# Performance work log

Measured on AMD Instinct MI355X. Metric: run time of the kernel, lower is better.

The kernel has to match this reference:

```python
import jax, jax.numpy as jnp
import numpy as np

B, T, D = 8, 512, 1024
H, DQK, DV = 16, 128, 128  # n_heads, d_qk = emb_dim//h_qk, d_v = emb_dim//h_v


def setup_inputs() -> dict:
    key = jax.random.key(0)
    ks = jax.random.split(key, 8)
    s = 0.02
    return {
        "X": jax.random.normal(ks[0], (B, T, D), jnp.float32),
        "pos_enc_k": jax.random.normal(ks[1], (T, T, DQK), jnp.float32) * s,
        "pos_enc_v": jax.random.normal(ks[2], (T, T, DV), jnp.float32) * s,
        "Wq": jax.random.normal(ks[3], (D, H * DQK), jnp.float32) * s,
        "bq": jnp.zeros((H * DQK,), jnp.float32),
        "Wk": jax.random.normal(ks[4], (D, H * DQK), jnp.float32) * s,
        "bk": jnp.zeros((H * DQK,), jnp.float32),
        "Wv": jax.random.normal(ks[5], (D, H * DV), jnp.float32) * s,
        "bv": jnp.zeros((H * DV,), jnp.float32),
        "Wp": jax.random.normal(ks[6], (H * DV, D), jnp.float32) * s,
        "bp": jnp.zeros((D,), jnp.float32),
    }


def reference(X, pos_enc_k, pos_enc_v, Wq, bq, Wk, bk, Wv, bv, Wp, bp):
    b, t, d = X.shape
    # projections -> (b, h, t, dhead)
    Q = (X @ Wq + bq).reshape(b, t, H, DQK).transpose(0, 2, 1, 3)
    K = (X @ Wk + bk).reshape(b, t, H, DQK).transpose(0, 2, 1, 3)
    V = (X @ Wv + bv).reshape(b, t, H, DV).transpose(0, 2, 1, 3)
    # content attention + relative-position key bias
    att = jnp.einsum("bhqd,bhkd->bhqk", Q, K)
    att = att + jnp.einsum("bhqd,qkd->bhqk", Q, pos_enc_k)
    att = att / jnp.sqrt(jnp.asarray(DQK, X.dtype))
    # causal mask (do_mask=True)
    causal = jnp.tril(jnp.ones((t, t), bool))
    att = jnp.where(causal[None, None], att, jnp.asarray(-jnp.inf, att.dtype))
    att = jax.nn.softmax(att, axis=-1)
    # values + relative-position value correction
    y = jnp.einsum("bhqk,bhkd->bhqd", att, V)
    y = y + jnp.einsum("bhqk,qkd->bhqd", att, pos_enc_v)
    y = y.transpose(0, 2, 1, 3).reshape(b, t, H * DV)
    return y @ Wp + bp
```

## Files before the change

### kernel.cpp

```cpp
#include <hip/hip_runtime.h>
#include <stdint.h>

#define B_  8
#define T_  512
#define D_  1024
#define H_  16
#define DH  128
#define BH  128
#define ND  2048
#define BT  4096

typedef __attribute__((ext_vector_type(8))) short          short8;
typedef __attribute__((ext_vector_type(8))) __bf16         bf16x8;
typedef __attribute__((ext_vector_type(4))) float          f32x4;
typedef __attribute__((ext_vector_type(4))) unsigned short ushort4v;

static __device__ __forceinline__ unsigned short f2bf(float f) {
  unsigned u = __builtin_bit_cast(unsigned, f);
  u += 0x7FFFu + ((u >> 16) & 1u);
  return (unsigned short)(u >> 16);
}
static __device__ __forceinline__ float bf2f(unsigned short h) {
  unsigned u = ((unsigned)h) << 16;
  return __builtin_bit_cast(float, u);
}
static __device__ __forceinline__ f32x4 mfma16(short8 a, short8 b, f32x4 c) {
  return __builtin_amdgcn_mfma_f32_16x16x32_bf16(
      __builtin_bit_cast(bf16x8, a), __builtin_bit_cast(bf16x8, b), c, 0, 0, 0);
}
static __device__ __forceinline__ void gload16(const unsigned short* g, unsigned short* l) {
  __builtin_amdgcn_global_load_lds(
      (const __attribute__((address_space(1))) void*)g,
      (__attribute__((address_space(3))) void*)l, 16, 0, 0);
}

template <int ROWS, int COLS>
static __device__ __forceinline__ void stage_gl2(unsigned short* lds,
                                                 const unsigned short* __restrict__ src,
                                                 long stride, int tid) {
  constexpr int CPR = COLS / 8;
#pragma unroll
  for (int it = 0; it < ROWS * COLS / 8 / 256; ++it) {
    int chunk = tid + it * 256;
    int r = chunk / CPR, c8 = (chunk % CPR) * 8;
    gload16(src + (long)r * stride + c8, lds + chunk * 8);
  }
}

template <int ROWS>
static __device__ __forceinline__ void stage_sw64(unsigned short* lds,
                                                  const unsigned short* __restrict__ src,
                                                  long stride, int tid) {
#pragma unroll
  for (int it = 0; it < ROWS / 32; ++it) {
    int n = tid + it * 256;
    int r = n >> 3, c = (n & 7) ^ (r & 7);
    gload16(src + (long)r * stride + c * 8, lds + n * 8);
  }
}

template <int MR, int NR>
static __device__ __forceinline__ void mfma_sw64(const unsigned short* As,
                                                 const unsigned short* Bs,
                                                 int a0, int b0, int lrow, int g,
                                                 f32x4 (*acc)[NR]) {
#pragma unroll
  for (int ks = 0; ks < 2; ++ks) {
    short8 a[MR], b[NR];
#pragma unroll
    for (int i = 0; i < MR; ++i) {
      int ra = a0 + i * 16 + lrow;
      int c = (ks * 4 + g) ^ (ra & 7);
      a[i] = *(const short8*)&As[ra * 64 + c * 8];
    }
#pragma unroll
    for (int j = 0; j < NR; ++j) {
      int rb = b0 + j * 16 + lrow;
      int c = (ks * 4 + g) ^ (rb & 7);
      b[j] = *(const short8*)&Bs[rb * 64 + c * 8];
    }
#pragma unroll
    for (int i = 0; i < MR; ++i)
#pragma unroll
      for (int j = 0; j < NR; ++j) acc[i][j] = mfma16(a[i], b[j], acc[i][j]);
  }
}

#define IDS4                             \
  const int tid  = threadIdx.x;          \
  const int lane = tid & 63;             \
  const int wid  = tid >> 6;             \
  const int lrow = lane & 15;            \
  const int lk8  = (lane >> 4) * 8;      \
  const int lr4  = (lane >> 4) * 4;      \
  const int lg   = lane >> 4;            \
  const int wm = wid >> 1, wn = wid & 1;

#define LTS 132
#define LTQ 68

__global__ __launch_bounds__(256) void k_prep(const float* __restrict__ X,
                                              unsigned short* __restrict__ Xb,
                                              const float* __restrict__ Wq,
                                              const float* __restrict__ Wk,
                                              const float* __restrict__ Wv,
                                              const float* __restrict__ Wp,
                                              unsigned short* __restrict__ WT,
                                              unsigned short* __restrict__ WpT) {
  __shared__ float tile[32][33];
  int bid = blockIdx.x;
  if (bid < 4096) {
    int i = bid * 256 + threadIdx.x;
    f32x4 v = ((const f32x4*)X)[i];
    ushort4v o;
    o.x = f2bf(v.x); o.y = f2bf(v.y); o.z = f2bf(v.z); o.w = f2bf(v.w);
    ((ushort4v*)Xb)[i] = o;
    return;
  }
  bid -= 4096;
  const int which = bid >> 11;
  const int local = bid & 2047;
  const float* in;
  unsigned short* outp;
  int R, C, bx, by;
  if (which < 3) {
    in = which == 0 ? Wq : (which == 1 ? Wk : Wv);
    outp = WT + (size_t)which * ND * D_;
    R = D_; C = ND; bx = local & 63; by = local >> 6;
  } else {
    in = Wp; outp = WpT;
    R = ND; C = D_; bx = local & 31; by = local >> 5;
  }
  int c0 = bx * 32, r0 = by * 32;
  int tx = threadIdx.x & 31, ty = threadIdx.x >> 5;
#pragma unroll
  for (int i = 0; i < 32; i += 8)
    tile[ty + i][tx] = in[(long)(r0 + ty + i) * C + (c0 + tx)];
  __syncthreads();
#pragma unroll
  for (int i = 0; i < 32; i += 8)
    outp[(long)(c0 + ty + i) * R + (r0 + tx)] = f2bf(tile[tx][ty + i]);
}

__global__ __launch_bounds__(256) void k_proj8(const unsigned short* __restrict__ Xb,
                                               const unsigned short* __restrict__ WT,
                                               const float* __restrict__ bq,
                                               const float* __restrict__ bk,
                                               const float* __restrict__ bv,
                                               unsigned short* __restrict__ Qb,
                                               unsigned short* __restrict__ Kb,
                                               unsigned short* __restrict__ Vt) {
  __shared__ unsigned short As[128 * 64], Bs[128 * 64];
  IDS4
  const int flat = blockIdx.x, xcd = flat & 7, local = flat >> 3;
  const int nt = xcd * 6 + (local % 6);
  const int mt = local / 6;
  const int m0 = mt * 128, n0 = nt * 128;

  f32x4 acc[4][4] = {};
  for (int kk = 0; kk < D_; kk += 64) {
    stage_sw64<128>(As, Xb + (long)m0 * D_ + kk, D_, tid);
    stage_sw64<128>(Bs, WT + (long)n0 * D_ + kk, D_, tid);
    __syncthreads();
    mfma_sw64<4, 4>(As, Bs, wm * 64, wn * 64, lrow, lg, acc);
    __syncthreads();
  }

  const int nb = n0 >> 11;
  const float* biasp = nb == 0 ? bq : (nb == 1 ? bk : bv);
  const int hcol = (n0 & 2047) >> 7;
  if (nb < 2) {
    unsigned short* dst = nb == 0 ? Qb : Kb;
#pragma unroll
    for (int i = 0; i < 4; ++i)
#pragma unroll
      for (int j = 0; j < 4; ++j) {
        int cc = (n0 & 2047) + wn * 64 + j * 16 + lrow;
        int dd = cc & 127;
        float bias = biasp[cc];
#pragma unroll
        for (int r = 0; r < 4; ++r) {
          int m = m0 + wm * 64 + i * 16 + lr4 + r;
          int bb = m >> 9, tt = m & (T_ - 1);
          dst[((long)(bb * H_ + hcol) * T_ + tt) * DH + dd] = f2bf(acc[i][j][r] + bias);
        }
      }
  } else {
#pragma unroll
    for (int i = 0; i < 4; ++i)
#pragma unroll
      for (int j = 0; j < 4; ++j) {
        int cc = (n0 & 2047) + wn * 64 + j * 16 + lrow;
        int dd = cc & 127;
        float bias = biasp[cc];
#pragma unroll
        for (int r = 0; r < 4; ++r) {
          int m = m0 + wm * 64 + i * 16 + lr4 + r;
          int bb = m >> 9, tt = m & (T_ - 1);
          Vt[((long)(bb * H_ + hcol) * DH + dd) * T_ + tt] = f2bf(acc[i][j][r] + bias);
        }
      }
  }
}

__global__ __launch_bounds__(256) void k_posk(const unsigned short* __restrict__ Qb,
                                              const float* __restrict__ Pk,
                                              unsigned short* __restrict__ att) {
  const int bid = blockIdx.x;
  const int q = (bid & 1) ? (T_ - 1 - (bid >> 1)) : (bid >> 1);
  const int ktiles = (q >> 6) + 1;
  __shared__ unsigned short As[128 * 128];
  __shared__ unsigned short Bs[2][64 * 136];
  IDS4
  {
    const unsigned short* src = Qb + (long)q * DH;
#pragma unroll
    for (int it = 0; it < 8; ++it) {
      int n = tid + it * 256;
      int r = n >> 4, c = (n & 15) ^ (r & 7);
      gload16(src + (long)r * (T_ * DH) + c * 8, As + n * 8);
    }
  }
  f32x4 pv[8];
  const float* psrc = Pk + (long)q * T_ * DH;
  auto loadPk = [&](int kt) {
#pragma unroll
    for (int it = 0; it < 8; ++it) {
      int chunk = tid + it * 256;
      int r = chunk >> 5, c4 = (chunk & 31) * 4;
      pv[it] = *(const f32x4*)(psrc + (long)(kt * 64 + r) * DH + c4);
    }
  };
  auto writeB = [&](int buf) {
#pragma unroll
    for (int it = 0; it < 8; ++it) {
      int chunk = tid + it * 256;
      int r = chunk >> 5, c4 = (chunk & 31) * 4;
      ushort4v o;
      o.x = f2bf(pv[it].x); o.y = f2bf(pv[it].y); o.z = f2bf(pv[it].z); o.w = f2bf(pv[it].w);
      *(ushort4v*)&Bs[buf][r * 136 + c4] = o;
    }
  };
  loadPk(0);
  asm volatile("s_waitcnt vmcnt(0)" ::: "memory");
  writeB(0);
  asm volatile("s_waitcnt lgkmcnt(0)" ::: "memory");
  __builtin_amdgcn_s_barrier();
  for (int kt = 0; kt < ktiles; ++kt) {
    const bool pre = (kt + 1 < ktiles);
    if (pre) loadPk(kt + 1);
    f32x4 acc[4][2] = {};
#pragma unroll
    for (int ks = 0; ks < 4; ++ks) {
      short8 a[4], b[2];
#pragma unroll
      for (int i = 0; i < 4; ++i) {
        int ra = wm * 64 + i * 16 + lrow;
        int c = (ks * 4 + lg) ^ (ra & 7);
        a[i] = *(const short8*)&As[ra * 128 + c * 8];
      }
#pragma unroll
      for (int j = 0; j < 2; ++j)
        b[j] = *(const short8*)&Bs[kt & 1][(wn * 32 + j * 16 + lrow) * 136 + ks * 32 + lk8];
#pragma unroll
      for (int i = 0; i < 4; ++i)
#pragma unroll
        for (int j = 0; j < 2; ++j)
          acc[i][j] = mfma16(a[i], b[j], acc[i][j]);
    }
    if (pre) {
      asm volatile("s_waitcnt vmcnt(0)" ::: "memory");
      writeB((kt + 1) & 1);
    }
#pragma unroll
    for (int i = 0; i < 4; ++i)
#pragma unroll
      for (int j = 0; j < 2; ++j) {
        int k = kt * 64 + wn * 32 + j * 16 + lrow;
#pragma unroll
        for (int r = 0; r < 4; ++r) {
          int bh = wm * 64 + i * 16 + lr4 + r;
          att[((long)q * BH + bh) * T_ + k] = f2bf(acc[i][j][r]);
        }
      }
    asm volatile("s_waitcnt lgkmcnt(0)" ::: "memory");
    __builtin_amdgcn_s_barrier();
  }
}

__global__ __launch_bounds__(256) void k_qkv(const unsigned short* __restrict__ Qb,
                                             const unsigned short* __restrict__ Kb,
                                             const unsigned short* __restrict__ Vt,
                                             unsigned short* __restrict__ att,
                                             float* __restrict__ Sinv,
                                             unsigned short* __restrict__ Ybb) {
  const int bh = blockIdx.x & 127, pr = blockIdx.x >> 7;
  __shared__ unsigned short Qs[64 * 128], Ks[64 * 128], Vs[128 * 64];
  __shared__ unsigned short Ps[64 * 72];
  __shared__ float lt[64 * LTQ];
  __shared__ float sInv[64];
  const int tid = threadIdx.x;
  const int lane = tid & 63, wid = tid >> 6;
  const int wm = wid >> 1, wn = wid & 1;
  const int lrow = lane & 15, lk8 = (lane >> 4) * 8, lr4 = (lane >> 4) * 4;
  const int row = tid >> 2, c0 = (tid & 3) * 16;
  const float scale = 0.08838834764831845f;
  const int b = bh >> 4, h = bh & 15;

  for (int pass = 0; pass < 2; ++pass) {
    const int qt = pass ? 7 - pr : pr;
    const int q0 = qt * 64, ktiles = qt + 1;
    const int qabs = q0 + row;
    unsigned short* arow = att + ((long)qabs * BH + bh) * T_;
    {
      const unsigned short* src = Qb + ((long)bh * T_ + q0) * DH;
#pragma unroll
      for (int it = 0; it < 4; ++it) {
        int n = tid + it * 256;
        int r = n >> 4, c = (n & 15) ^ (r & 7);
        gload16(src + (long)r * DH + c * 8, Qs + n * 8);
      }
    }
    float ssum = 0.f;
    f32x4 accv[2][4] = {};
    for (int kt = 0; kt < ktiles; ++kt) {
      const unsigned short* ksrc = Kb + ((long)bh * T_ + kt * 64) * DH;
#pragma unroll
      for (int it = 0; it < 4; ++it) {
        int n = tid + it * 256;
        int r = n >> 4, c = (n & 15) ^ (r & 7);
        gload16(ksrc + (long)r * DH + c * 8, Ks + n * 8);
      }
      const unsigned short* vsrc = Vt + (long)bh * DH * T_ + kt * 64;
#pragma unroll
      for (int it = 0; it < 4; ++it) {
        int n = tid + it * 256;
        int r = n >> 3, c = (n & 7) ^ (r & 7);
        gload16(vsrc + (long)r * T_ + c * 8, Vs + n * 8);
      }
      short8 pb0 = *(const short8*)(arow + kt * 64 + c0);
      short8 pb1 = *(const short8*)(arow + kt * 64 + c0 + 8);
      __syncthreads();
      f32x4 acc[2][2] = {};
#pragma unroll
      for (int ks = 0; ks < 4; ++ks) {
        short8 aq[2], bk2[2];
#pragma unroll
        for (int i = 0; i < 2; ++i) {
          int ra = wm * 32 + i * 16 + lrow;
          int c = (ks * 4 + (lane >> 4)) ^ (ra & 7);
          aq[i] = *(const short8*)&Qs[ra * 128 + c * 8];
        }
#pragma unroll
        for (int j = 0; j < 2; ++j) {
          int rb = wn * 32 + j * 16 + lrow;
          int c = (ks * 4 + (lane >> 4)) ^ (rb & 7);
          bk2[j] = *(const short8*)&Ks[rb * 128 + c * 8];
        }
#pragma unroll
        for (int i = 0; i < 2; ++i)
#pragma unroll
          for (int j = 0; j < 2; ++j)
            acc[i][j] = mfma16(aq[i], bk2[j], acc[i][j]);
      }
#pragma unroll
      for (int i = 0; i < 2; ++i)
#pragma unroll
        for (int j = 0; j < 2; ++j)
#pragma unroll
          for (int r = 0; r < 4; ++r)
            lt[(wm * 32 + i * 16 + lr4 + r) * LTQ + wn * 32 + j * 16 + lrow] = acc[i][j][r];
      __syncthreads();
      short8 o0, o1;
#pragma unroll
      for (int jj = 0; jj < 8; ++jj) {
        int k = kt * 64 + c0 + jj;
        float e0 = (k <= qabs)
                   ? __expf((lt[row * LTQ + c0 + jj] + bf2f((unsigned short)pb0[jj])) * scale) : 0.f;
        float e1 = (k + 8 <= qabs)
                   ? __expf((lt[row * LTQ + c0 + 8 + jj] + bf2f((unsigned short)pb1[jj])) * scale) : 0.f;
        o0[jj] = (short)f2bf(e0);
        o1[jj] = (short)f2bf(e1);
        ssum += e0 + e1;
      }
      *(short8*)(arow + kt * 64 + c0) = o0;
      *(short8*)(arow + kt * 64 + c0 + 8) = o1;
      *(short8*)&Ps[row * 72 + c0] = o0;
      *(short8*)&Ps[row * 72 + c0 + 8] = o1;
      __syncthreads();
#pragma unroll
      for (int ks = 0; ks < 2; ++ks) {
        short8 ap[2], bv2[4];
#pragma unroll
        for (int i = 0; i < 2; ++i) {
          int ra = wm * 32 + i * 16 + lrow;
          ap[i] = *(const short8*)&Ps[ra * 72 + ks * 32 + lk8];
        }
#pragma unroll
        for (int j = 0; j < 4; ++j) {
          int rb = wn * 64 + j * 16 + lrow;
          int c = ((ks * 4) + (lane >> 4)) ^ (rb & 7);
          bv2[j] = *(const short8*)&Vs[rb * 64 + c * 8];
        }
#pragma unroll
        for (int i = 0; i < 2; ++i)
#pragma unroll
          for (int j = 0; j < 4; ++j)
            accv[i][j] = mfma16(ap[i], bv2[j], accv[i][j]);
      }
      __syncthreads();
    }
    ssum += __shfl_xor(ssum, 1, 64);
    ssum += __shfl_xor(ssum, 2, 64);
    float si = 1.f / ssum;
    if ((tid & 3) == 0) { sInv[row] = si; Sinv[(long)qabs * BH + bh] = si; }
    __syncthreads();
#pragma unroll
    for (int i = 0; i < 2; ++i) {
      float sc2[4];
#pragma unroll
      for (int r = 0; r < 4; ++r) sc2[r] = sInv[wm * 32 + i * 16 + lr4 + r];
#pragma unroll
      for (int j = 0; j < 4; ++j) {
        int d = wn * 64 + j * 16 + lrow;
#pragma unroll
        for (int r = 0; r < 4; ++r) {
          int q = q0 + wm * 32 + i * 16 + lr4 + r;
          Ybb[(long)(b * T_ + q) * ND + h * DH + d] = f2bf(accv[i][j][r] * sc2[r]);
        }
      }
    }
    __syncthreads();
  }
}

__global__ __launch_bounds__(256) void k_posv(const unsigned short* __restrict__ P,
                                              const float* __restrict__ Pv,
                                              const float* __restrict__ Sinv,
                                              unsigned short* __restrict__ Ybb) {
  const int bid = blockIdx.x;
  const int q = (bid & 1) ? (T_ - 1 - (bid >> 1)) : (bid >> 1);
  const int ktiles = (q >> 6) + 1;
  __shared__ unsigned short As[128 * 64];
  __shared__ unsigned short Bs[2][128 * 72];
  __shared__ float lt[64 * LTQ];
  IDS4
  f32x4 pv[8];
  const float* psrc = Pv + (long)q * T_ * DH;
  auto loadPv = [&](int kt) {
#pragma unroll
    for (int it = 0; it < 8; ++it) {
      int chunk = tid + it * 256;
      int d4 = (chunk & 3) * 4 + ((chunk >> 6) & 7) * 16;
      int k  = ((chunk >> 2) & 15) + ((chunk >> 9) & 3) * 16;
      pv[it] = *(const f32x4*)(psrc + (long)(kt * 64 + k) * DH + d4);
    }
  };
  auto writeB = [&](int buf) {
#pragma unroll
    for (int it = 0; it < 8; ++it) {
      int chunk = tid + it * 256;
      int d4 = (chunk & 3) * 4 + ((chunk >> 6) & 7) * 16;
      int k  = ((chunk >> 2) & 15) + ((chunk >> 9) & 3) * 16;
      Bs[buf][(d4 + 0) * 72 + k] = f2bf(pv[it].x);
      Bs[buf][(d4 + 1) * 72 + k] = f2bf(pv[it].y);
      Bs[buf][(d4 + 2) * 72 + k] = f2bf(pv[it].z);
      Bs[buf][(d4 + 3) * 72 + k] = f2bf(pv[it].w);
    }
  };
  loadPv(0);
  asm volatile("s_waitcnt vmcnt(0)" ::: "memory");
  writeB(0);
  asm volatile("s_waitcnt lgkmcnt(0)" ::: "memory");
  __builtin_amdgcn_s_barrier();
  f32x4 acc[4][4] = {};
  for (int kt = 0; kt < ktiles; ++kt) {
    const bool pre = (kt + 1 < ktiles);
    stage_sw64<128>(As, P + (long)q * BH * T_ + kt * 64, T_, tid);
    if (pre) loadPv(kt + 1);
    if (pre) asm volatile("s_waitcnt vmcnt(8)" ::: "memory");
    else     asm volatile("s_waitcnt vmcnt(0)" ::: "memory");
    __builtin_amdgcn_s_barrier();
#pragma unroll
    for (int ks = 0; ks < 2; ++ks) {
      short8 a[4], b[4];
#pragma unroll
      for (int i = 0; i < 4; ++i) {
        int ra = wm * 64 + i * 16 + lrow;
        int c = (ks * 4 + lg) ^ (ra & 7);
        a[i] = *(const short8*)&As[ra * 64 + c * 8];
      }
#pragma unroll
      for (int j = 0; j < 4; ++j)
        b[j] = *(const short8*)&Bs[kt & 1][(wn * 64 + j * 16 + lrow) * 72 + ks * 32 + lk8];
#pragma unroll
      for (int i = 0; i < 4; ++i)
#pragma unroll
        for (int j = 0; j < 4; ++j)
          acc[i][j] = mfma16(a[i], b[j], acc[i][j]);
    }
    if (pre) {
      asm volatile("s_waitcnt vmcnt(0)" ::: "memory");
      writeB((kt + 1) & 1);
    }
    asm volatile("s_waitcnt lgkmcnt(0)" ::: "memory");
    __builtin_amdgcn_s_barrier();
  }
  const int row = tid >> 2, c0 = (tid & 3) * 16;
#pragma unroll
  for (int hb = 0; hb < 2; ++hb)
#pragma unroll
    for (int hd = 0; hd < 2; ++hd) {
      int bh = hb * 64 + row;
      long idx = ((long)((bh >> 4) * T_ + q)) * ND + (bh & 15) * DH + hd * 64 + c0;
      short8 y0 = *(const short8*)&Ybb[idx];
      short8 y1 = *(const short8*)&Ybb[idx + 8];
      float sc = Sinv[(long)q * BH + bh];
      if (wm == hb && wn == hd) {
#pragma unroll
        for (int i = 0; i < 4; ++i)
#pragma unroll
          for (int j = 0; j < 4; ++j)
#pragma unroll
            for (int r = 0; r < 4; ++r)
              lt[(i * 16 + lr4 + r) * LTQ + j * 16 + lrow] = acc[i][j][r];
      }
      __syncthreads();
      short8 o0, o1;
#pragma unroll
      for (int jj = 0; jj < 8; ++jj) {
        o0[jj] = (short)f2bf(lt[row * LTQ + c0 + jj] * sc + bf2f((unsigned short)y0[jj]));
        o1[jj] = (short)f2bf(lt[row * LTQ + c0 + 8 + jj] * sc + bf2f((unsigned short)y1[jj]));
      }
      *(short8*)&Ybb[idx] = o0;
      *(short8*)&Ybb[idx + 8] = o1;
      __syncthreads();
    }
}

__global__ __launch_bounds__(256) void k_oproj(const unsigned short* __restrict__ Ybb,
                                               const unsigned short* __restrict__ WpT,
                                               const float* __restrict__ bp,
                                               float* __restrict__ outp) {
  __shared__ unsigned short As[128 * 64], Bs[128 * 64];
  IDS4
  const int m0 = blockIdx.y * 128, n0 = blockIdx.x * 128;
  f32x4 acc[4][4] = {};
  for (int kk = 0; kk < ND; kk += 64) {
    stage_sw64<128>(As, Ybb + (long)m0 * ND + kk, ND, tid);
    stage_sw64<128>(Bs, WpT + (long)n0 * ND + kk, ND, tid);
    __syncthreads();
    mfma_sw64<4, 4>(As, Bs, wm * 64, wn * 64, lrow, lg, acc);
    __syncthreads();
  }
  float* lt = (float*)As;
  const int row = tid >> 4, c8 = (tid & 15) * 8;
  f32x4 b0 = *(const f32x4*)(bp + n0 + c8);
  f32x4 b1 = *(const f32x4*)(bp + n0 + c8 + 4);
#pragma unroll
  for (int rr = 0; rr < 8; ++rr) {
    if (wm == (rr >> 2)) {
      const int ii = rr & 3;
#pragma unroll
      for (int j = 0; j < 4; ++j)
#pragma unroll
        for (int r = 0; r < 4; ++r)
          lt[(lr4 + r) * LTS + wn * 64 + j * 16 + lrow] = acc[ii][j][r];
    }
    __syncthreads();
    f32x4 v0 = *(const f32x4*)&lt[row * LTS + c8];
    f32x4 v1 = *(const f32x4*)&lt[row * LTS + c8 + 4];
    int m = m0 + rr * 16 + row;
    v0.x += b0.x; v0.y += b0.y; v0.z += b0.z; v0.w += b0.w;
    v1.x += b1.x; v1.y += b1.y; v1.z += b1.z; v1.w += b1.w;
    *(f32x4*)&outp[(long)m * D_ + n0 + c8] = v0;
    *(f32x4*)&outp[(long)m * D_ + n0 + c8 + 4] = v1;
    __syncthreads();
  }
}

extern "C" void kernel_launch(void* const* d_in, const int* in_sizes, int n_in,
                              void* d_out, int out_size, void* d_ws, size_t ws_size,
                              hipStream_t stream) {
  const float* X  = (const float*)d_in[0];
  const float* Pk = (const float*)d_in[1];
  const float* Pv = (const float*)d_in[2];
  const float* Wq = (const float*)d_in[3];
  const float* bq = (const float*)d_in[4];
  const float* Wk = (const float*)d_in[5];
  const float* bk = (const float*)d_in[6];
  const float* Wv = (const float*)d_in[7];
  const float* bv = (const float*)d_in[8];
  const float* Wp = (const float*)d_in[9];
  const float* bp = (const float*)d_in[10];
  float* out = (float*)d_out;

  uint8_t* w = (uint8_t*)d_ws;
  unsigned short* Xb  = (unsigned short*)w; w += (size_t)BT * D_ * 2;
  unsigned short* WT  = (unsigned short*)w; w += (size_t)3 * ND * D_ * 2;
  unsigned short* WpT = (unsigned short*)w; w += (size_t)D_ * ND * 2;
  unsigned short* Qb  = (unsigned short*)w; w += (size_t)BH * T_ * DH * 2;
  unsigned short* Kb  = (unsigned short*)w; w += (size_t)BH * T_ * DH * 2;
  unsigned short* Vt  = (unsigned short*)w; w += (size_t)BH * DH * T_ * 2;
  unsigned short* att = (unsigned short*)w; w += (size_t)T_ * BH * T_ * 2;
  unsigned short* Ybb = (unsigned short*)w; w += (size_t)BT * ND * 2;
  float*          Sinv= (float*)w;          w += (size_t)T_ * BH * 4;

  k_prep<<<12288, 256, 0, stream>>>(X, Xb, Wq, Wk, Wv, Wp, WT, WpT);
  k_proj8<<<1536, 256, 0, stream>>>(Xb, WT, bq, bk, bv, Qb, Kb, Vt);
  k_posk<<<T_, 256, 0, stream>>>(Qb, Pk, att);
  k_qkv<<<512, 256, 0, stream>>>(Qb, Kb, Vt, att, Sinv, Ybb);
  k_posv<<<T_, 256, 0, stream>>>(att, Pv, Sinv, Ybb);
  k_oproj<<<dim3(D_ / 128, BT / 128), 256, 0, stream>>>(Ybb, WpT, bp, out);
}
```

Measured before the change: 238.4 us.

## Prefetch next K/V and P tiles with double buffering in attention kernels

In the attention kernel, Q fragments are now loaded straight into registers instead of being staged through LDS. V is double-buffered, and the next tile's K and V loads are issued right after the QK scores are written, so they overlap the softmax and PV work. The posv kernel double-buffers the P tile and issues the next tile's loads before the current MFMA work, waiting only for the older batch. This hides global-load latency behind compute at the cost of more LDS and registers per block, which may lower occupancy.

```diff
diff --git a/kernel.cpp b/kernel.cpp
--- a/kernel.cpp
+++ b/kernel.cpp
@@ -32,19 +32,6 @@
   __builtin_amdgcn_global_load_lds(
       (const __attribute__((address_space(1))) void*)g,
       (__attribute__((address_space(3))) void*)l, 16, 0, 0);
-}
-
-template <int ROWS, int COLS>
-static __device__ __forceinline__ void stage_gl2(unsigned short* lds,
-                                                 const unsigned short* __restrict__ src,
-                                                 long stride, int tid) {
-  constexpr int CPR = COLS / 8;
-#pragma unroll
-  for (int it = 0; it < ROWS * COLS / 8 / 256; ++it) {
-    int chunk = tid + it * 256;
-    int r = chunk / CPR, c8 = (chunk % CPR) * 8;
-    gload16(src + (long)r * stride + c8, lds + chunk * 8);
-  }
 }
 
 template <int ROWS>
@@ -295,7 +282,8 @@
                                              float* __restrict__ Sinv,
                                              unsigned short* __restrict__ Ybb) {
   const int bh = blockIdx.x & 127, pr = blockIdx.x >> 7;
-  __shared__ unsigned short Qs[64 * 128], Ks[64 * 128], Vs[128 * 64];
+  __shared__ unsigned short Ks[64 * 128];
+  __shared__ unsigned short Vs[2][128 * 64];
   __shared__ unsigned short Ps[64 * 72];
   __shared__ float lt[64 * LTQ];
   __shared__ float sInv[64];
@@ -307,50 +295,51 @@
   const float scale = 0.08838834764831845f;
   const int b = bh >> 4, h = bh & 15;
 
+  auto stageK = [&](int kt) {
+    const unsigned short* ksrc = Kb + ((long)bh * T_ + kt * 64) * DH;
+#pragma unroll
+    for (int it = 0; it < 4; ++it) {
+      int n = tid + it * 256;
+      int r = n >> 4, c = (n & 15) ^ (r & 7);
+      gload16(ksrc + (long)r * DH + c * 8, Ks + n * 8);
+    }
+  };
+  auto stageV = [&](int kt, int buf) {
+    const unsigned short* vsrc = Vt + (long)bh * DH * T_ + kt * 64;
+#pragma unroll
+    for (int it = 0; it < 4; ++it) {
+      int n = tid + it * 256;
+      int r = n >> 3, c = (n & 7) ^ (r & 7);
+      gload16(vsrc + (long)r * T_ + c * 8, Vs[buf] + n * 8);
+    }
+  };
+
   for (int pass = 0; pass < 2; ++pass) {
     const int qt = pass ? 7 - pr : pr;
     const int q0 = qt * 64, ktiles = qt + 1;
     const int qabs = q0 + row;
     unsigned short* arow = att + ((long)qabs * BH + bh) * T_;
-    {
-      const unsigned short* src = Qb + ((long)bh * T_ + q0) * DH;
-#pragma unroll
-      for (int it = 0; it < 4; ++it) {
-        int n = tid + it * 256;
-        int r = n >> 4, c = (n & 15) ^ (r & 7);
-        gload16(src + (long)r * DH + c * 8, Qs + n * 8);
-      }
-    }
+    short8 aq[2][4];
+#pragma unroll
+    for (int i = 0; i < 2; ++i)
+#pragma unroll
+      for (int ks = 0; ks < 4; ++ks)
+        aq[i][ks] = *(const short8*)&Qb[((long)bh * T_ + q0 + wm * 32 + i * 16 + lrow) * DH + ks * 32 + lk8];
+    stageK(0); stageV(0, 0);
+    asm volatile("s_waitcnt vmcnt(0)" ::: "memory");
+    __builtin_amdgcn_sched_barrier(0);
+    __builtin_amdgcn_s_barrier();
     float ssum = 0.f;
     f32x4 accv[2][4] = {};
+    int cur = 0;
     for (int kt = 0; kt < ktiles; ++kt) {
-      const unsigned short* ksrc = Kb + ((long)bh * T_ + kt * 64) * DH;
-#pragma unroll
-      for (int it = 0; it < 4; ++it) {
-        int n = tid + it * 256;
-        int r = n >> 4, c = (n & 15) ^ (r & 7);
-        gload16(ksrc + (long)r * DH + c * 8, Ks + n * 8);
-      }
-      const unsigned short* vsrc = Vt + (long)bh * DH * T_ + kt * 64;
-#pragma unroll
-      for (int it = 0; it < 4; ++it) {
-        int n = tid + it * 256;
-        int r = n >> 3, c = (n & 7) ^ (r & 7);
-        gload16(vsrc + (long)r * T_ + c * 8, Vs + n * 8);
-      }
+      const bool pre = (kt + 1 < ktiles);
       short8 pb0 = *(const short8*)(arow + kt * 64 + c0);
       short8 pb1 = *(const short8*)(arow + kt * 64 + c0 + 8);
-      __syncthreads();
       f32x4 acc[2][2] = {};
 #pragma unroll
       for (int ks = 0; ks < 4; ++ks) {
-        short8 aq[2], bk2[2];
-#pragma unroll
-        for (int i = 0; i < 2; ++i) {
-          int ra = wm * 32 + i * 16 + lrow;
-          int c = (ks * 4 + (lane >> 4)) ^ (ra & 7);
-          aq[i] = *(const short8*)&Qs[ra * 128 + c * 8];
-        }
+        short8 bk2[2];
 #pragma unroll
         for (int j = 0; j < 2; ++j) {
           int rb = wn * 32 + j * 16 + lrow;
@@ -361,7 +350,7 @@
         for (int i = 0; i < 2; ++i)
 #pragma unroll
           for (int j = 0; j < 2; ++j)
-            acc[i][j] = mfma16(aq[i], bk2[j], acc[i][j]);
+            acc[i][j] = mfma16(aq[i][ks], bk2[j], acc[i][j]);
       }
 #pragma unroll
       for (int i = 0; i < 2; ++i)
@@ -370,7 +359,10 @@
 #pragma unroll
           for (int r = 0; r < 4; ++r)
             lt[(wm * 32 + i * 16 + lr4 + r) * LTQ + wn * 32 + j * 16 + lrow] = acc[i][j][r];
-      __syncthreads();
+      asm volatile("s_waitcnt lgkmcnt(0)" ::: "memory");
+      __builtin_amdgcn_sched_barrier(0);
+      __builtin_amdgcn_s_barrier();
+      if (pre) { stageK(kt + 1); stageV(kt + 1, cur ^ 1); }
       short8 o0, o1;
 #pragma unroll
       for (int jj = 0; jj < 8; ++jj) {
@@ -387,7 +379,9 @@
       *(short8*)(arow + kt * 64 + c0 + 8) = o1;
       *(short8*)&Ps[row * 72 + c0] = o0;
       *(short8*)&Ps[row * 72 + c0 + 8] = o1;
-      __syncthreads();
+      asm volatile("s_waitcnt lgkmcnt(0)" ::: "memory");
+      __builtin_amdgcn_sched_barrier(0);
+      __builtin_amdgcn_s_barrier();
 #pragma unroll
       for (int ks = 0; ks < 2; ++ks) {
         short8 ap[2], bv2[4];
@@ -400,7 +394,7 @@
         for (int j = 0; j < 4; ++j) {
           int rb = wn * 64 + j * 16 + lrow;
           int c = ((ks * 4) + (lane >> 4)) ^ (rb & 7);
-          bv2[j] = *(const short8*)&Vs[rb * 64 + c * 8];
+          bv2[j] = *(const short8*)&Vs[cur][rb * 64 + c * 8];
         }
 #pragma unroll
         for (int i = 0; i < 2; ++i)
@@ -408,7 +402,11 @@
           for (int j = 0; j < 4; ++j)
             accv[i][j] = mfma16(ap[i], bv2[j], accv[i][j]);
       }
-      __syncthreads();
+      if (pre) asm volatile("s_waitcnt vmcnt(0)" ::: "memory");
+      asm volatile("s_waitcnt lgkmcnt(0)" ::: "memory");
+      __builtin_amdgcn_sched_barrier(0);
+      __builtin_amdgcn_s_barrier();
+      cur ^= 1;
     }
     ssum += __shfl_xor(ssum, 1, 64);
     ssum += __shfl_xor(ssum, 2, 64);
@@ -441,7 +439,7 @@
   const int bid = blockIdx.x;
   const int q = (bid & 1) ? (T_ - 1 - (bid >> 1)) : (bid >> 1);
   const int ktiles = (q >> 6) + 1;
-  __shared__ unsigned short As[128 * 64];
+  __shared__ unsigned short As[2][128 * 64];
   __shared__ unsigned short Bs[2][128 * 72];
   __shared__ float lt[64 * LTQ];
   IDS4
@@ -468,6 +466,7 @@
       Bs[buf][(d4 + 3) * 72 + k] = f2bf(pv[it].w);
     }
   };
+  stage_sw64<128>(As[0], P + (long)q * BH * T_, T_, tid);
   loadPv(0);
   asm volatile("s_waitcnt vmcnt(0)" ::: "memory");
   writeB(0);
@@ -476,10 +475,13 @@
   f32x4 acc[4][4] = {};
   for (int kt = 0; kt < ktiles; ++kt) {
     const bool pre = (kt + 1 < ktiles);
-    stage_sw64<128>(As, P + (long)q * BH * T_ + kt * 64, T_, tid);
-    if (pre) loadPv(kt + 1);
-    if (pre) asm volatile("s_waitcnt vmcnt(8)" ::: "memory");
-    else     asm volatile("s_waitcnt vmcnt(0)" ::: "memory");
+    if (pre) {
+      stage_sw64<128>(As[(kt + 1) & 1], P + (long)q * BH * T_ + (kt + 1) * 64, T_, tid);
+      loadPv(kt + 1);
+      asm volatile("s_waitcnt vmcnt(12)" ::: "memory");
+    } else {
+      asm volatile("s_waitcnt vmcnt(0)" ::: "memory");
+    }
     __builtin_amdgcn_s_barrier();
 #pragma unroll
     for (int ks = 0; ks < 2; ++ks) {
@@ -488,7 +490,7 @@
       for (int i = 0; i < 4; ++i) {
         int ra = wm * 64 + i * 16 + lrow;
         int c = (ks * 4 + lg) ^ (ra & 7);
-        a[i] = *(const short8*)&As[ra * 64 + c * 8];
+        a[i] = *(const short8*)&As[kt & 1][ra * 64 + c * 8];
       }
 #pragma unroll
       for (int j = 0; j < 4; ++j)
@@ -499,10 +501,7 @@
         for (int j = 0; j < 4; ++j)
           acc[i][j] = mfma16(a[i], b[j], acc[i][j]);
     }
-    if (pre) {
-      asm volatile("s_waitcnt vmcnt(0)" ::: "memory");
-      writeB((kt + 1) & 1);
-    }
+    if (pre) writeB((kt + 1) & 1);
     asm volatile("s_waitcnt lgkmcnt(0)" ::: "memory");
     __builtin_amdgcn_s_barrier();
   }
```

Result: slower. 245.1 us (+2.8%).
